# Optimization experiments

Measured on AMD Instinct MI355X. Metric: run time of the kernel, lower is better.

Reference implementation:

```python
import jax, jax.numpy as jnp
import numpy as np

NUM_HID = 512

def setup_inputs() -> dict:
    key = jax.random.key(0)
    k_x, k_w1, k_b1, k_w2, k_b2 = jax.random.split(key, 5)
    x = jax.random.normal(k_x, (1000000, 2), dtype=jnp.float32)
    # PyTorch nn.Linear init: U(-1/sqrt(fan_in), 1/sqrt(fan_in))
    lim1 = 1.0 / np.sqrt(2.0)
    W1 = jax.random.uniform(k_w1, (NUM_HID, 2), jnp.float32, -lim1, lim1)
    b1 = jax.random.uniform(k_b1, (NUM_HID,), jnp.float32, -lim1, lim1)
    lim2 = 1.0 / np.sqrt(NUM_HID)
    W2 = jax.random.uniform(k_w2, (1, NUM_HID), jnp.float32, -lim2, lim2)
    b2 = jax.random.uniform(k_b2, (1,), jnp.float32, -lim2, lim2)
    return {"x": x, "W1": W1, "b1": b1, "W2": W2, "b2": b2}

def reference(x, W1, b1, W2, b2):
    # Polar conversion: r = sqrt(x^2 + y^2), theta = atan2(y, x) -- fused, vectorized
    r = jnp.sqrt(x[:, 0] ** 2 + x[:, 1] ** 2)
    theta = jnp.arctan2(x[:, 1], x[:, 0])
    polar = jnp.stack([r, theta], axis=-1)            # [N, 2]
    h = jnp.tanh(polar @ W1.T + b1)                    # [N, H]
    out = jax.nn.sigmoid(h @ W2.T + b2)                # [N, 1]
    return out
```

## Files before the change

### kernel.cpp

```cpp
#include <hip/hip_runtime.h>

#define NHID  512
#define BLK_B 256
#define BLK_E 512
#define NR    128
#define NT    128
#define RMAX  7.0f
#define PI_F  3.14159265358979323846f
#define LOG2E 1.44269504088896340736f

#define Q4C  0.00047410f
#define Q3C -0.0091865f
#define Q2C  0.070220f
#define Q1C -0.292009f
#define Q0C  0.994707f
#define XCLAMP 2.6f

__global__ __launch_bounds__(BLK_B) void build_table(
    const float2* __restrict__ W1, const float* __restrict__ b1,
    const float*  __restrict__ W2, const float* __restrict__ b2,
    float* __restrict__ table)
{
    __shared__ float4 wq[NHID];
    const int t = threadIdx.x;

    #pragma unroll
    for (int j = t; j < NHID; j += BLK_B) {
        const float2 w = W1[j];
        wq[8 * (j & 63) + (j >> 6)] = make_float4(w.x, w.y, b1[j], W2[j]);
    }
    __syncthreads();

    const int node = blockIdx.x * (BLK_B / 8) + (t >> 3);
    const int q    = t & 7;
    const int ir = node & (NR - 1);
    const int it = node >> 7;
    const float r  = (float)ir * (RMAX / (float)(NR - 1));
    const float th = -PI_F + (float)it * (2.0f * PI_F / (float)(NT - 1));

    float acc = 0.0f;
    #pragma unroll 8
    for (int i = 0; i < NHID / 8; ++i) {
        const float4 w = wq[8 * i + q];
        float a = fmaf(w.x, r, fmaf(w.y, th, w.z));
        a = fminf(fmaxf(a, -XCLAMP), XCLAMP);
        const float u = a * a;
        float p = fmaf(Q4C, u, Q3C);
        p = fmaf(p, u, Q2C);
        p = fmaf(p, u, Q1C);
        p = fmaf(p, u, Q0C);
        acc = fmaf(w.w * a, p, acc);
    }
    acc += __shfl_xor(acc, 1);
    acc += __shfl_xor(acc, 2);
    acc += __shfl_xor(acc, 4);
    if (q == 0) table[node] = acc + b2[0];
}

__global__ __launch_bounds__(BLK_E) void polar_eval(
    const float2* __restrict__ x, const float* __restrict__ table,
    float* __restrict__ out, int N)
{
    __shared__ float Tl[NT * NR];
    const int t = threadIdx.x;

    {
        const float4* Tg = (const float4*)table;
        float4* Ts = (float4*)Tl;
        #pragma unroll
        for (int k = t; k < NT * NR / 4; k += BLK_E) Ts[k] = Tg[k];
    }
    __syncthreads();

    const int base = blockIdx.x * (BLK_E * 4) + t;
    #pragma unroll
    for (int kq = 0; kq < 4; ++kq) {
        const int i = base + kq * BLK_E;
        if (i >= N) continue;
        const float2 p = x[i];

        const float r = __builtin_amdgcn_sqrtf(fmaf(p.x, p.x, p.y * p.y));

        const float ax = fabsf(p.x), ay = fabsf(p.y);
        const float mx = fmaxf(ax, ay), mn = fminf(ax, ay);
        const float tt = mn * __builtin_amdgcn_rcpf(mx);
        const float z2 = tt * tt;
        float at = fmaf(z2, 0.0208351f, -0.0851330f);
        at = fmaf(at, z2, 0.1801410f);
        at = fmaf(at, z2, -0.3302995f);
        at = fmaf(at, z2, 0.9998660f);
        at *= tt;
        at = (ay > ax)   ? (0.5f * PI_F - at) : at;
        at = (p.x < 0.f) ? (PI_F - at)        : at;
        at = copysignf(at, p.y);

        float u = fminf(r * ((float)(NR - 1) / RMAX), (float)(NR - 1) - 0.001f);
        float v = fminf(fmaxf((at + PI_F) * ((float)(NT - 1) / (2.0f * PI_F)), 0.0f),
                        (float)(NT - 1) - 0.001f);
        const float fu = floorf(u), fv = floorf(v);
        const int iu = (int)fu, iv = (int)fv;
        const float du = u - fu, dv = v - fv;
        const int idx = iv * NR + iu;
        const float f00 = Tl[idx],      f01 = Tl[idx + 1];
        const float f10 = Tl[idx + NR], f11 = Tl[idx + NR + 1];
        const float a0 = fmaf(du, f01 - f00, f00);
        const float a1 = fmaf(du, f11 - f10, f10);
        const float z  = fmaf(dv, a1 - a0, a0);

        const float ez = __builtin_amdgcn_exp2f(-z * LOG2E);
        out[i] = __builtin_amdgcn_rcpf(1.0f + ez);
    }
}

__global__ __launch_bounds__(256) void polar_direct(
    const float2* __restrict__ x, const float2* __restrict__ W1,
    const float* __restrict__ b1, const float* __restrict__ W2,
    const float* __restrict__ b2, float* __restrict__ out, int N)
{
    __shared__ float4 wq[NHID];
    const int t = threadIdx.x;
    const float c = 2.0f * LOG2E;
    #pragma unroll
    for (int j = t; j < NHID; j += 256) {
        const float2 w = W1[j];
        wq[j] = make_float4(w.x * c, w.y * c, b1[j] * c, W2[j]);
    }
    __syncthreads();

    const int i = blockIdx.x * 256 + t;
    if (i >= N) return;
    const float2 p = x[i];
    const float r  = __builtin_amdgcn_sqrtf(fmaf(p.x, p.x, p.y * p.y));
    const float th = atan2f(p.y, p.x);
    float acc = b2[0];
    #pragma unroll 4
    for (int j = 0; j < NHID; ++j) {
        const float4 w = wq[j];
        const float a = fmaf(w.x, r, fmaf(w.y, th, w.z));
        const float e = __builtin_amdgcn_exp2f(a);
        const float th_ = fmaf(-2.0f, __builtin_amdgcn_rcpf(e + 1.0f), 1.0f);
        acc = fmaf(w.w, th_, acc);
    }
    const float ez = __builtin_amdgcn_exp2f(-acc * LOG2E);
    out[i] = __builtin_amdgcn_rcpf(1.0f + ez);
}

extern "C" void kernel_launch(void* const* d_in, const int* in_sizes, int n_in,
                              void* d_out, int out_size, void* d_ws, size_t ws_size,
                              hipStream_t stream) {
    const float* x  = (const float*)d_in[0];
    const float* W1 = (const float*)d_in[1];
    const float* b1 = (const float*)d_in[2];
    const float* W2 = (const float*)d_in[3];
    const float* b2 = (const float*)d_in[4];
    float* out = (float*)d_out;
    const int N = in_sizes[0] / 2;

    if (ws_size >= (size_t)NT * NR * sizeof(float)) {
        float* table = (float*)d_ws;
        build_table<<<(NT * NR) / (BLK_B / 8), BLK_B, 0, stream>>>(
            (const float2*)W1, b1, W2, b2, table);
        polar_eval<<<(N + BLK_E * 4 - 1) / (BLK_E * 4), BLK_E, 0, stream>>>(
            (const float2*)x, table, out, N);
    } else {
        polar_direct<<<(N + 255) / 256, 256, 0, stream>>>(
            (const float2*)x, (const float2*)W1, b1, W2, b2, out, N);
    }
}
```

Measured before the change: 71.98 us.

## Fuse table build and evaluation into one cooperative kernel with grid sync

Merges the table-building kernel and the polar evaluation kernel into a single cooperative launch of 256 blocks of 512 threads. A grid-wide barrier separates the two phases, and shared memory is reused for both the weights and the table. Each block now processes 8 points per thread instead of 4, so fewer blocks each copy the 64KB table into LDS. This removes one kernel launch and the inter-kernel gap, at the cost of the grid-sync overhead, cooperative-launch restrictions, and a fixed grid that must cover N.

```diff
diff --git a/kernel.cpp b/kernel.cpp
--- a/kernel.cpp
+++ b/kernel.cpp
@@ -1,8 +1,11 @@
 #include <hip/hip_runtime.h>
+#include <hip/hip_cooperative_groups.h>
+
+namespace cg = cooperative_groups;
 
 #define NHID  512
-#define BLK_B 256
-#define BLK_E 512
+#define BLK   512
+#define GRID  256
 #define NR    128
 #define NT    128
 #define RMAX  7.0f
@@ -16,66 +19,65 @@
 #define Q0C  0.994707f
 #define XCLAMP 2.6f
 
-__global__ __launch_bounds__(BLK_B) void build_table(
+__global__ __launch_bounds__(BLK) void polar_all(
+    const float2* __restrict__ x,
     const float2* __restrict__ W1, const float* __restrict__ b1,
     const float*  __restrict__ W2, const float* __restrict__ b2,
-    float* __restrict__ table)
+    float* __restrict__ table, float* __restrict__ out, int N)
 {
-    __shared__ float4 wq[NHID];
+    __shared__ float Tl[NT * NR];
+    float4* wq = (float4*)Tl;
+
     const int t = threadIdx.x;
 
-    #pragma unroll
-    for (int j = t; j < NHID; j += BLK_B) {
-        const float2 w = W1[j];
-        wq[8 * (j & 63) + (j >> 6)] = make_float4(w.x, w.y, b1[j], W2[j]);
+    {
+        const float2 w = W1[t];
+        wq[8 * (t & 63) + (t >> 6)] = make_float4(w.x, w.y, b1[t], W2[t]);
     }
     __syncthreads();
 
-    const int node = blockIdx.x * (BLK_B / 8) + (t >> 3);
-    const int q    = t & 7;
-    const int ir = node & (NR - 1);
-    const int it = node >> 7;
-    const float r  = (float)ir * (RMAX / (float)(NR - 1));
-    const float th = -PI_F + (float)it * (2.0f * PI_F / (float)(NT - 1));
+    {
+        const int q    = t & 7;
+        const int node = blockIdx.x * (BLK / 8) + (t >> 3);
+        const int ir = node & (NR - 1);
+        const int it = node >> 7;
+        const float r  = (float)ir * (RMAX / (float)(NR - 1));
+        const float th = -PI_F + (float)it * (2.0f * PI_F / (float)(NT - 1));
 
-    float acc = 0.0f;
-    #pragma unroll 8
-    for (int i = 0; i < NHID / 8; ++i) {
-        const float4 w = wq[8 * i + q];
-        float a = fmaf(w.x, r, fmaf(w.y, th, w.z));
-        a = fminf(fmaxf(a, -XCLAMP), XCLAMP);
-        const float u = a * a;
-        float p = fmaf(Q4C, u, Q3C);
-        p = fmaf(p, u, Q2C);
-        p = fmaf(p, u, Q1C);
-        p = fmaf(p, u, Q0C);
-        acc = fmaf(w.w * a, p, acc);
+        float acc = 0.0f;
+        #pragma unroll 8
+        for (int i = 0; i < NHID / 8; ++i) {
+            const float4 w = wq[8 * i + q];
+            float a = fmaf(w.x, r, fmaf(w.y, th, w.z));
+            a = fminf(fmaxf(a, -XCLAMP), XCLAMP);
+            const float u = a * a;
+            float p = fmaf(Q4C, u, Q3C);
+            p = fmaf(p, u, Q2C);
+            p = fmaf(p, u, Q1C);
+            p = fmaf(p, u, Q0C);
+            acc = fmaf(w.w * a, p, acc);
+        }
+        acc += __shfl_xor(acc, 1);
+        acc += __shfl_xor(acc, 2);
+        acc += __shfl_xor(acc, 4);
+        if (q == 0) table[node] = acc + b2[0];
     }
-    acc += __shfl_xor(acc, 1);
-    acc += __shfl_xor(acc, 2);
-    acc += __shfl_xor(acc, 4);
-    if (q == 0) table[node] = acc + b2[0];
-}
 
-__global__ __launch_bounds__(BLK_E) void polar_eval(
-    const float2* __restrict__ x, const float* __restrict__ table,
-    float* __restrict__ out, int N)
-{
-    __shared__ float Tl[NT * NR];
-    const int t = threadIdx.x;
+    __threadfence();
+    cg::this_grid().sync();
 
     {
         const float4* Tg = (const float4*)table;
         float4* Ts = (float4*)Tl;
         #pragma unroll
-        for (int k = t; k < NT * NR / 4; k += BLK_E) Ts[k] = Tg[k];
+        for (int k = t; k < NT * NR / 4; k += BLK) Ts[k] = Tg[k];
     }
     __syncthreads();
 
-    const int base = blockIdx.x * (BLK_E * 4) + t;
+    const int base = blockIdx.x * (BLK * 8) + t;
     #pragma unroll
-    for (int kq = 0; kq < 4; ++kq) {
-        const int i = base + kq * BLK_E;
+    for (int kq = 0; kq < 8; ++kq) {
+        const int i = base + kq * BLK;
         if (i >= N) continue;
         const float2 p = x[i];
 
@@ -148,22 +150,22 @@
 extern "C" void kernel_launch(void* const* d_in, const int* in_sizes, int n_in,
                               void* d_out, int out_size, void* d_ws, size_t ws_size,
                               hipStream_t stream) {
-    const float* x  = (const float*)d_in[0];
-    const float* W1 = (const float*)d_in[1];
-    const float* b1 = (const float*)d_in[2];
-    const float* W2 = (const float*)d_in[3];
-    const float* b2 = (const float*)d_in[4];
+    const float2* x  = (const float2*)d_in[0];
+    const float2* W1 = (const float2*)d_in[1];
+    const float*  b1 = (const float*)d_in[2];
+    const float*  W2 = (const float*)d_in[3];
+    const float*  b2 = (const float*)d_in[4];
     float* out = (float*)d_out;
-    const int N = in_sizes[0] / 2;
+    int N = in_sizes[0] / 2;
 
     if (ws_size >= (size_t)NT * NR * sizeof(float)) {
         float* table = (float*)d_ws;
-        build_table<<<(NT * NR) / (BLK_B / 8), BLK_B, 0, stream>>>(
-            (const float2*)W1, b1, W2, b2, table);
-        polar_eval<<<(N + BLK_E * 4 - 1) / (BLK_E * 4), BLK_E, 0, stream>>>(
-            (const float2*)x, table, out, N);
+        void* args[] = { (void*)&x, (void*)&W1, (void*)&b1, (void*)&W2,
+                         (void*)&b2, (void*)&table, (void*)&out, (void*)&N };
+        hipLaunchCooperativeKernel(reinterpret_cast<void*>(polar_all),
+                                   dim3(GRID), dim3(BLK), args, 0, stream);
     } else {
         polar_direct<<<(N + 255) / 256, 256, 0, stream>>>(
-            (const float2*)x, (const float2*)W1, b1, W2, b2, out, N);
+            x, W1, b1, W2, b2, out, N);
     }
 }
```

Measured after the change: 130.9 us. 1.82x slower.
